# Kernel optimization log

Hardware: AMD Instinct MI355X
Metric: run time of the kernel (lower is better)

The kernel has to match this reference:

```python
import jax, jax.numpy as jnp
import numpy as np

E = 100000          # number of edges
IN_FEATS = 256      # in_edge_feats
HIDDEN = 128        # hidden_size
K = 16              # neighbors per edge (uniform-degree rendering of ragged lists)


def setup_inputs() -> dict:
    key = jax.random.key(0)
    k1, k2, k3, k4 = jax.random.split(key, 4)
    edge_feats = jax.random.normal(k1, (E, IN_FEATS), dtype=jnp.float32)
    neighbors = jax.random.randint(k2, (E, K), 0, E, dtype=jnp.int32)
    # Linear params (torch Linear: y = x @ W^T + b; here W stored as [in, out])
    W = jax.random.normal(k3, (IN_FEATS, HIDDEN), dtype=jnp.float32) / np.sqrt(IN_FEATS)
    b = jax.random.normal(k4, (HIDDEN,), dtype=jnp.float32) * 0.01
    return {"edge_feats": edge_feats, "neighbors": neighbors, "W": W, "b": b}


def reference(edge_feats, neighbors, W, b):
    # Dense linear transform of all edge features: [E, H]
    t = edge_feats @ W + b
    # Gather each edge's K neighbor transformed features and sum: [E, K, H] -> [E, H]
    nbr_sum = jnp.take(t, neighbors, axis=0).sum(axis=1)
    # agg[i] = t[i] + sum_{n in neighbors[i]} t[n]
    return t + nbr_sum
```

## Files before the change

kernel.cpp:

```cpp
#include <hip/hip_runtime.h>
#include <hip/hip_bf16.h>
#include <stdint.h>

#define E_EDGES 100000
#define IN_F    256
#define HID     128
#define KNB     16

typedef short bf16x8 __attribute__((ext_vector_type(8)));
typedef float f32x4  __attribute__((ext_vector_type(4)));

__device__ __forceinline__ unsigned short f2bf(float f) {
    union { float f; unsigned u; } v; v.f = f;
    unsigned u = v.u;
    u += 0x7fffu + ((u >> 16) & 1u);
    return (unsigned short)(u >> 16);
}

__global__ void conv_w_kernel(const float* __restrict__ W, unsigned short* __restrict__ Wt) {
    int t = blockIdx.x * blockDim.x + threadIdx.x;
    int n = t & (HID - 1);
    int k = t >> 7;
    Wt[(size_t)n * IN_F + k] = f2bf(W[(size_t)k * HID + n]);
}

__launch_bounds__(256)
__global__ void gemm_t_kernel(const float* __restrict__ A,
                              const unsigned short* __restrict__ Wt,
                              const float* __restrict__ bias,
                              unsigned short* __restrict__ T) {
    const int wave = threadIdx.x >> 6;
    const int lane = threadIdx.x & 63;
    const int l15  = lane & 15;
    const int quad = lane >> 4;
    const int rowbase = blockIdx.x * 64 + wave * 16;

    int arow = rowbase + l15;
    if (arow >= E_EDGES) arow = E_EDGES - 1;

    const float* ap = A + (size_t)arow * IN_F + quad * 8;
    float4 apre[16];
    #pragma unroll
    for (int k0 = 0; k0 < 8; ++k0) {
        apre[2 * k0]     = *(const float4*)(ap + k0 * 32);
        apre[2 * k0 + 1] = *(const float4*)(ap + k0 * 32 + 4);
    }

    f32x4 acc[8] = {};

    #pragma unroll
    for (int k0 = 0; k0 < 8; ++k0) {
        bf16x8 bfrag[8];
        #pragma unroll
        for (int ct = 0; ct < 8; ++ct)
            bfrag[ct] = *(const bf16x8*)(Wt + (size_t)(ct * 16 + l15) * IN_F
                                            + k0 * 32 + quad * 8);
        float4 lo = apre[2 * k0], hi = apre[2 * k0 + 1];
        bf16x8 af;
        af[0] = (short)f2bf(lo.x); af[1] = (short)f2bf(lo.y);
        af[2] = (short)f2bf(lo.z); af[3] = (short)f2bf(lo.w);
        af[4] = (short)f2bf(hi.x); af[5] = (short)f2bf(hi.y);
        af[6] = (short)f2bf(hi.z); af[7] = (short)f2bf(hi.w);
        #pragma unroll
        for (int ct = 0; ct < 8; ++ct)
            acc[ct] = __builtin_amdgcn_mfma_f32_16x16x32_bf16(af, bfrag[ct], acc[ct], 0, 0, 0);
    }

    #pragma unroll
    for (int ct = 0; ct < 8; ++ct) {
        const int col = ct * 16 + l15;
        const float bv = bias[col];
        #pragma unroll
        for (int i = 0; i < 4; ++i) {
            const int row = rowbase + quad * 4 + i;
            if (row < E_EDGES)
                T[(size_t)row * HID + col] = f2bf(acc[ct][i] + bv);
        }
    }
}

__launch_bounds__(256)
__global__ void gather_sum_kernel(const unsigned short* __restrict__ T,
                                  const int* __restrict__ nbr,
                                  float* __restrict__ out) {
    __shared__ int sidx[256];
    const int tid   = threadIdx.x;
    const int edge0 = blockIdx.x * 16;
    sidx[tid] = nbr[(size_t)edge0 * KNB + tid];
    __syncthreads();

    const int el   = tid >> 4;
    const int lane = tid & 15;
    const int edge = edge0 + el;

    float acc[8];
    {
        uint4 v = *(const uint4*)(T + (size_t)edge * HID + lane * 8);
        unsigned w[4] = { v.x, v.y, v.z, v.w };
        union { unsigned u; float f; } c;
        #pragma unroll
        for (int j = 0; j < 4; ++j) {
            c.u = w[j] << 16;          acc[2 * j]     = c.f;
            c.u = w[j] & 0xffff0000u;  acc[2 * j + 1] = c.f;
        }
    }
    #pragma unroll
    for (int k = 0; k < KNB; ++k) {
        const int n = sidx[el * KNB + k];
        uint4 v = *(const uint4*)(T + (size_t)n * HID + lane * 8);
        unsigned w[4] = { v.x, v.y, v.z, v.w };
        union { unsigned u; float f; } c;
        #pragma unroll
        for (int j = 0; j < 4; ++j) {
            c.u = w[j] << 16;          acc[2 * j]     += c.f;
            c.u = w[j] & 0xffff0000u;  acc[2 * j + 1] += c.f;
        }
    }

    float* op = out + (size_t)edge * HID + lane * 8;
    float4 o0 = { acc[0], acc[1], acc[2], acc[3] };
    float4 o1 = { acc[4], acc[5], acc[6], acc[7] };
    *(float4*)op       = o0;
    *(float4*)(op + 4) = o1;
}

extern "C" void kernel_launch(void* const* d_in, const int* in_sizes, int n_in,
                              void* d_out, int out_size, void* d_ws, size_t ws_size,
                              hipStream_t stream) {
    const float* edge_feats = (const float*)d_in[0];
    const int*   neighbors  = (const int*)d_in[1];
    const float* W          = (const float*)d_in[2];
    const float* b          = (const float*)d_in[3];
    float*       out        = (float*)d_out;

    unsigned short* Wt = (unsigned short*)d_ws;
    unsigned short* T  = (unsigned short*)d_ws + (size_t)IN_F * HID;

    conv_w_kernel<<<(IN_F * HID) / 256, 256, 0, stream>>>(W, Wt);
    gemm_t_kernel<<<(E_EDGES + 63) / 64, 256, 0, stream>>>(edge_feats, Wt, b, T);
    gather_sum_kernel<<<E_EDGES / 16, 256, 0, stream>>>(T, neighbors, out);
}
```

Baseline: 268.4 us.

## Pre-convert activations to bf16 and stage W fragments in shared memory

Adds a separate kernel that converts edge_feats to bf16 into the output buffer, used as scratch. The GEMM then reads half-width activations and stages the whole transposed weight (64KB) into LDS in an MFMA-fragment-friendly layout instead of re-reading it from global for every wave. The extra pass re-reads the fp32 input and writes a bf16 copy, and the per-block 64KB LDS load limits occupancy.

```diff
diff --git a/kernel.cpp b/kernel.cpp
--- a/kernel.cpp
+++ b/kernel.cpp
@@ -25,45 +25,60 @@
 }
 
 __launch_bounds__(256)
-__global__ void gemm_t_kernel(const float* __restrict__ A,
+__global__ void conv_a_kernel(const float* __restrict__ A, unsigned short* __restrict__ Abf) {
+    size_t i = ((size_t)blockIdx.x * 256 + threadIdx.x) * 8;
+    float4 lo = *(const float4*)(A + i);
+    float4 hi = *(const float4*)(A + i + 4);
+    uint4 o;
+    o.x = (unsigned)f2bf(lo.x) | ((unsigned)f2bf(lo.y) << 16);
+    o.y = (unsigned)f2bf(lo.z) | ((unsigned)f2bf(lo.w) << 16);
+    o.z = (unsigned)f2bf(hi.x) | ((unsigned)f2bf(hi.y) << 16);
+    o.w = (unsigned)f2bf(hi.z) | ((unsigned)f2bf(hi.w) << 16);
+    *(uint4*)(Abf + i) = o;
+}
+
+__launch_bounds__(256)
+__global__ void gemm_t_kernel(const unsigned short* __restrict__ Abf,
                               const unsigned short* __restrict__ Wt,
                               const float* __restrict__ bias,
                               unsigned short* __restrict__ T) {
-    const int wave = threadIdx.x >> 6;
-    const int lane = threadIdx.x & 63;
+    __shared__ unsigned short Bs[32768];
+    const int tid = threadIdx.x;
+
+    #pragma unroll
+    for (int it = 0; it < 16; ++it) {
+        int e    = it * 256 + tid;
+        int n    = e >> 5;
+        int k8   = e & 31;
+        int dst  = ((k8 >> 2) * 8 + (n >> 4)) * 64 + (k8 & 3) * 16 + (n & 15);
+        uint4 v = *(const uint4*)(Wt + (size_t)e * 8);
+        *(uint4*)(Bs + (size_t)dst * 8) = v;
+    }
+
+    const int wave = tid >> 6;
+    const int lane = tid & 63;
     const int l15  = lane & 15;
     const int quad = lane >> 4;
     const int rowbase = blockIdx.x * 64 + wave * 16;
-
     int arow = rowbase + l15;
     if (arow >= E_EDGES) arow = E_EDGES - 1;
 
-    const float* ap = A + (size_t)arow * IN_F + quad * 8;
-    float4 apre[16];
+    const unsigned short* ap = Abf + (size_t)arow * IN_F + quad * 8;
+    bf16x8 apre[8];
+    #pragma unroll
+    for (int k0 = 0; k0 < 8; ++k0)
+        apre[k0] = *(const bf16x8*)(ap + k0 * 32);
+
+    __syncthreads();
+
+    f32x4 acc[8] = {};
     #pragma unroll
     for (int k0 = 0; k0 < 8; ++k0) {
-        apre[2 * k0]     = *(const float4*)(ap + k0 * 32);
-        apre[2 * k0 + 1] = *(const float4*)(ap + k0 * 32 + 4);
-    }
-
-    f32x4 acc[8] = {};
-
-    #pragma unroll
-    for (int k0 = 0; k0 < 8; ++k0) {
-        bf16x8 bfrag[8];
         #pragma unroll
-        for (int ct = 0; ct < 8; ++ct)
-            bfrag[ct] = *(const bf16x8*)(Wt + (size_t)(ct * 16 + l15) * IN_F
-                                            + k0 * 32 + quad * 8);
-        float4 lo = apre[2 * k0], hi = apre[2 * k0 + 1];
-        bf16x8 af;
-        af[0] = (short)f2bf(lo.x); af[1] = (short)f2bf(lo.y);
-        af[2] = (short)f2bf(lo.z); af[3] = (short)f2bf(lo.w);
-        af[4] = (short)f2bf(hi.x); af[5] = (short)f2bf(hi.y);
-        af[6] = (short)f2bf(hi.z); af[7] = (short)f2bf(hi.w);
-        #pragma unroll
-        for (int ct = 0; ct < 8; ++ct)
-            acc[ct] = __builtin_amdgcn_mfma_f32_16x16x32_bf16(af, bfrag[ct], acc[ct], 0, 0, 0);
+        for (int ct = 0; ct < 8; ++ct) {
+            bf16x8 bf = *(const bf16x8*)(Bs + ((size_t)((k0 * 8 + ct) * 64 + lane)) * 8);
+            acc[ct] = __builtin_amdgcn_mfma_f32_16x16x32_bf16(apre[k0], bf, acc[ct], 0, 0, 0);
+        }
     }
 
     #pragma unroll
@@ -133,10 +148,12 @@
     const float* b          = (const float*)d_in[3];
     float*       out        = (float*)d_out;
 
-    unsigned short* Wt = (unsigned short*)d_ws;
-    unsigned short* T  = (unsigned short*)d_ws + (size_t)IN_F * HID;
+    unsigned short* Wt  = (unsigned short*)d_ws;
+    unsigned short* T   = (unsigned short*)d_ws + (size_t)IN_F * HID;
+    unsigned short* Abf = (unsigned short*)d_out;
 
     conv_w_kernel<<<(IN_F * HID) / 256, 256, 0, stream>>>(W, Wt);
-    gemm_t_kernel<<<(E_EDGES + 63) / 64, 256, 0, stream>>>(edge_feats, Wt, b, T);
+    conv_a_kernel<<<(E_EDGES * IN_F) / (256 * 8), 256, 0, stream>>>(edge_feats, Abf);
+    gemm_t_kernel<<<(E_EDGES + 63) / 64, 256, 0, stream>>>(Abf, Wt, b, T);
     gather_sum_kernel<<<E_EDGES / 16, 256, 0, stream>>>(T, neighbors, out);
 }
```

After: 264.3 us. About the same (-1.5%).
